# Kernel tuning notes

Hardware: AMD Instinct MI355X
Metric: run time of the kernel (lower is better)

Reference implementation:

```python
import jax, jax.numpy as jnp
import numpy as np

B, T, E, H = 4, 4096, 1024, 64

def setup_inputs() -> dict:
    key = jax.random.key(0)
    k1, k2, k3, k4 = jax.random.split(key, 4)
    embeddings = jax.random.normal(k1, (B, T, E), dtype=jnp.float32)
    Wq = jax.random.normal(k2, (H, E), dtype=jnp.float32) * (1.0 / np.sqrt(E))
    Wk = jax.random.normal(k3, (H, E), dtype=jnp.float32) * (1.0 / np.sqrt(E))
    Wv = jax.random.normal(k4, (H, E), dtype=jnp.float32) * (1.0 / np.sqrt(E))
    return {"embeddings": embeddings, "Wq": Wq, "Wk": Wk, "Wv": Wv}

def reference(embeddings, Wq, Wk, Wv):
    # Linear(E, H, bias=False): x @ W.T, W: [H, E]
    q = jnp.einsum('bte,he->bth', embeddings, Wq)  # [B,T,H]
    k = jnp.einsum('bte,he->bth', embeddings, Wk)  # [B,T,H]
    v = jnp.einsum('bte,he->bth', embeddings, Wv)  # [B,T,H]
    scale = embeddings.shape[-1] ** -0.5  # NOTE: source scales by embed_size**-0.5
    wei = jnp.einsum('bqh,bkh->bqk', q, k) * scale  # [B,T,T]
    Tn = embeddings.shape[1]
    causal = jnp.tril(jnp.ones((Tn, Tn), dtype=bool))
    wei = jnp.where(causal[None, :, :], wei, -jnp.inf)
    wei = jax.nn.softmax(wei, axis=-1)
    return jnp.einsum('bqk,bkh->bqh', wei, v)  # [B,T,H]
```

## Files before the change

### kernel.cpp

```cpp
#include <hip/hip_runtime.h>
#include <math.h>
#include <stdint.h>

#define BN 4
#define TN 4096
#define EN 1024
#define HN 64
#define BT (BN*TN)

typedef __attribute__((ext_vector_type(8))) short   short8;
typedef __attribute__((ext_vector_type(4))) float   f32x4;
typedef __attribute__((ext_vector_type(4))) unsigned short us4;
typedef __attribute__((ext_vector_type(8))) unsigned short us8;

__device__ __forceinline__ unsigned short f2b(float f) {
    union { float f; uint32_t u; } v; v.f = f;
    uint32_t u = v.u;
    return (unsigned short)((u + 0x7FFFu + ((u >> 16) & 1u)) >> 16);
}

__device__ __forceinline__ float fexp2(float x) {
#if __has_builtin(__builtin_amdgcn_exp2f)
    return __builtin_amdgcn_exp2f(x);
#else
    return exp2f(x);
#endif
}

__global__ __launch_bounds__(256)
void wconv(const float* __restrict__ Wq, const float* __restrict__ Wk,
           const float* __restrict__ Wv, unsigned short* __restrict__ W16) {
    const int row = blockIdx.x;
    const int t = threadIdx.x;
    const float* src;
    float sc = 1.0f;
    if (row < 64)       { src = Wq + (size_t)row * EN; sc = 0.045084220f; }
    else if (row < 128) { src = Wk + (size_t)(row - 64) * EN; }
    else                { src = Wv + (size_t)(row - 128) * EN; }
    float4 v = *(const float4*)(src + t * 4);
    us4 p;
    p[0] = f2b(v.x * sc); p[1] = f2b(v.y * sc);
    p[2] = f2b(v.z * sc); p[3] = f2b(v.w * sc);
    *(us4*)&W16[(size_t)row * EN + t * 4] = p;
}

__global__ __launch_bounds__(512, 2)
void qkv_gemm(const float* __restrict__ emb, const unsigned short* __restrict__ W16,
              unsigned short* __restrict__ QK, unsigned short* __restrict__ VT) {
    __shared__ __align__(16) unsigned short A_lds[2][64][72];
    __shared__ __align__(16) unsigned short B_lds[2][192][72];

    const int tid = threadIdx.x;
    const int wid = tid >> 6, lane = tid & 63;
    const int c = lane & 15, g = lane >> 4;
    const int wm = wid & 1, wn = wid >> 1;
    const int r0 = blockIdx.x * 64;

    const int ar = tid >> 3, ach = tid & 7;

    const f32x4 fzero = {0.f, 0.f, 0.f, 0.f};
    f32x4 acc[2][3];
    #pragma unroll
    for (int i = 0; i < 2; ++i)
        #pragma unroll
        for (int j = 0; j < 3; ++j) acc[i][j] = fzero;

    {
        float4 a0 = *(const float4*)&emb[(size_t)(r0 + ar) * EN + ach * 8];
        float4 a1 = *(const float4*)&emb[(size_t)(r0 + ar) * EN + ach * 8 + 4];
        us8 ap;
        ap[0] = f2b(a0.x); ap[1] = f2b(a0.y); ap[2] = f2b(a0.z); ap[3] = f2b(a0.w);
        ap[4] = f2b(a1.x); ap[5] = f2b(a1.y); ap[6] = f2b(a1.z); ap[7] = f2b(a1.w);
        *(us8*)&A_lds[0][ar][ach * 8] = ap;
        #pragma unroll
        for (int s = 0; s < 3; ++s) {
            const int f = tid + 512 * s;
            const int br = f >> 3, bch = f & 7;
            *(us8*)&B_lds[0][br][bch * 8] = *(const us8*)&W16[(size_t)br * EN + bch * 8];
        }
    }
    __syncthreads();

    for (int t = 0; t < 16; ++t) {
        const int cur = t & 1;
        const bool pf = (t < 15);
        const int kn = (t + 1) * 64;

        float4 a0, a1;
        us8 bw0, bw1, bw2;
        if (pf) {
            a0 = *(const float4*)&emb[(size_t)(r0 + ar) * EN + kn + ach * 8];
            a1 = *(const float4*)&emb[(size_t)(r0 + ar) * EN + kn + ach * 8 + 4];
            bw0 = *(const us8*)&W16[(size_t)((tid +    0) >> 3) * EN + kn + (tid & 7) * 8];
            bw1 = *(const us8*)&W16[(size_t)((tid +  512) >> 3) * EN + kn + ((tid + 512) & 7) * 8];
            bw2 = *(const us8*)&W16[(size_t)((tid + 1024) >> 3) * EN + kn + ((tid + 1024) & 7) * 8];
        }

        short8 af[2][2], bf[3][2];
        #pragma unroll
        for (int rt = 0; rt < 2; ++rt)
            #pragma unroll
            for (int ks = 0; ks < 2; ++ks)
                af[rt][ks] = *(const short8*)&A_lds[cur][32 * wm + 16 * rt + c][32 * ks + 8 * g];
        #pragma unroll
        for (int nt = 0; nt < 3; ++nt)
            #pragma unroll
            for (int ks = 0; ks < 2; ++ks)
                bf[nt][ks] = *(const short8*)&B_lds[cur][48 * wn + 16 * nt + c][32 * ks + 8 * g];
        #pragma unroll
        for (int ks = 0; ks < 2; ++ks)
            #pragma unroll
            for (int rt = 0; rt < 2; ++rt)
                #pragma unroll
                for (int nt = 0; nt < 3; ++nt)
                    acc[rt][nt] = __builtin_amdgcn_mfma_f32_16x16x32_bf16(
                        af[rt][ks], bf[nt][ks], acc[rt][nt], 0, 0, 0);

        if (pf) {
            us8 ap;
            ap[0] = f2b(a0.x); ap[1] = f2b(a0.y); ap[2] = f2b(a0.z); ap[3] = f2b(a0.w);
            ap[4] = f2b(a1.x); ap[5] = f2b(a1.y); ap[6] = f2b(a1.z); ap[7] = f2b(a1.w);
            *(us8*)&A_lds[cur ^ 1][ar][ach * 8] = ap;
            *(us8*)&B_lds[cur ^ 1][(tid +    0) >> 3][((tid +    0) & 7) * 8] = bw0;
            *(us8*)&B_lds[cur ^ 1][(tid +  512) >> 3][((tid +  512) & 7) * 8] = bw1;
            *(us8*)&B_lds[cur ^ 1][(tid + 1024) >> 3][((tid + 1024) & 7) * 8] = bw2;
        }
        __syncthreads();
    }

    #pragma unroll
    for (int rt = 0; rt < 2; ++rt) {
        #pragma unroll
        for (int nt = 0; nt < 3; ++nt) {
            const int n = 48 * wn + 16 * nt + c;
            const int wsel = n >> 6;
            const int d = n & 63;
            const int rbase = r0 + 32 * wm + 16 * rt + 4 * g;
            if (wsel < 2) {
                #pragma unroll
                for (int j = 0; j < 4; ++j)
                    QK[(size_t)wsel * BT * HN + (size_t)(rbase + j) * HN + d] =
                        f2b(acc[rt][nt][j]);
            } else {
                const int bb = rbase >> 12;
                const int tt = rbase & 4095;
                us4 p;
                #pragma unroll
                for (int j = 0; j < 4; ++j) p[j] = f2b(acc[rt][nt][j]);
                *(us4*)&VT[(size_t)bb * HN * TN + (size_t)d * TN + tt] = p;
            }
        }
    }
}

#define NW 4

__global__ __launch_bounds__(256, 2)
void attn(const unsigned short* __restrict__ QK,
          const unsigned short* __restrict__ VT, float* __restrict__ out) {
    __shared__ __align__(16) unsigned short KV[NW][2][64][72];
    __shared__ __align__(16) float MLm[NW][32];
    __shared__ __align__(16) float MLl[NW][32];
    __shared__ __align__(16) float ML2m[32];
    __shared__ __align__(16) float ML2l[32];

    const int tid = threadIdx.x;
    const int w = tid >> 6, lane = tid & 63, c = lane & 15, g = lane >> 4;
    const int bid = blockIdx.x;
    const int b = bid & 3;
    const int qt = (TN / 32 - 1) - (bid >> 2);

    const unsigned short* Qg = QK + ((size_t)b * TN + (size_t)qt * 32) * HN;
    const unsigned short* Kg = QK + (size_t)BT * HN + (size_t)b * TN * HN;
    const unsigned short* Vg = VT + (size_t)b * HN * TN;

    short8 bq[2][2];
    #pragma unroll
    for (int ct = 0; ct < 2; ++ct)
        #pragma unroll
        for (int ks = 0; ks < 2; ++ks)
            bq[ct][ks] = *(const short8*)&Qg[(size_t)(16 * ct + c) * HN + 32 * ks + 8 * g];

    const f32x4 fzero = {0.f, 0.f, 0.f, 0.f};
    f32x4 o[2][4];
    #pragma unroll
    for (int i = 0; i < 2; ++i)
        #pragma unroll
        for (int j = 0; j < 4; ++j) o[i][j] = fzero;
    float m[2] = {-INFINITY, -INFINITY};
    float l[2] = {0.f, 0.f};

    const int jmax = qt >> 1;
    unsigned short* Ks = &KV[w][0][0][0];
    unsigned short* Vs = &KV[w][1][0][0];

    for (int jt = w; jt <= jmax; jt += NW) {
        #pragma unroll
        for (int i = 0; i < 8; ++i) {
            const int f = lane + 64 * i;
            const int r = f >> 3, ch = f & 7;
            *(us8*)&Ks[r * 72 + ch * 8] =
                *(const us8*)&Kg[((size_t)jt * 64 + r) * HN + ch * 8];
        }
        #pragma unroll
        for (int i = 0; i < 8; ++i) {
            const int f = lane + 64 * i;
            const int r = f >> 3, ch = f & 7;
            *(us8*)&Vs[r * 72 + ch * 8] =
                *(const us8*)&Vg[(size_t)r * TN + (size_t)jt * 64 + ch * 8];
        }

        f32x4 st[4][2];
        #pragma unroll
        for (int kt = 0; kt < 4; ++kt)
            #pragma unroll
            for (int ct = 0; ct < 2; ++ct) st[kt][ct] = fzero;
        #pragma unroll
        for (int kt = 0; kt < 4; ++kt) {
            #pragma unroll
            for (int ks = 0; ks < 2; ++ks) {
                short8 ak = *(const short8*)&Ks[(16 * kt + c) * 72 + 32 * ks + 8 * g];
                #pragma unroll
                for (int ct = 0; ct < 2; ++ct)
                    st[kt][ct] = __builtin_amdgcn_mfma_f32_16x16x32_bf16(
                        ak, bq[ct][ks], st[kt][ct], 0, 0, 0);
            }
        }

        if (jt == jmax) {
            const int koff = jt * 64 - qt * 32;
            #pragma unroll
            for (int kt = 0; kt < 4; ++kt)
                #pragma unroll
                for (int ct = 0; ct < 2; ++ct)
                    #pragma unroll
                    for (int j = 0; j < 4; ++j)
                        if (16 * kt + 4 * g + j + koff > 16 * ct + c)
                            st[kt][ct][j] = -INFINITY;
        }

        #pragma unroll
        for (int ct = 0; ct < 2; ++ct) {
            float pmax = -INFINITY;
            #pragma unroll
            for (int kt = 0; kt < 4; ++kt)
                #pragma unroll
                for (int j = 0; j < 4; ++j) pmax = fmaxf(pmax, st[kt][ct][j]);
            pmax = fmaxf(pmax, __shfl_xor(pmax, 16));
            pmax = fmaxf(pmax, __shfl_xor(pmax, 32));
            const float mn = fmaxf(m[ct], pmax);
            const float alpha = fexp2(m[ct] - mn);
            float ls = 0.f;
            #pragma unroll
            for (int kt = 0; kt < 4; ++kt)
                #pragma unroll
                for (int j = 0; j < 4; ++j) {
                    float p = fexp2(st[kt][ct][j] - mn);
                    st[kt][ct][j] = p;
                    ls += p;
                }
            ls += __shfl_xor(ls, 16);
            ls += __shfl_xor(ls, 32);
            l[ct] = l[ct] * alpha + ls;
            m[ct] = mn;

            float a4[4];
            #pragma unroll
            for (int j = 0; j < 4; ++j) a4[j] = __shfl(alpha, 4 * g + j);
            #pragma unroll
            for (int dt = 0; dt < 4; ++dt)
                #pragma unroll
                for (int j = 0; j < 4; ++j) o[ct][dt][j] *= a4[j];
        }

        #pragma unroll
        for (int kt = 0; kt < 4; ++kt)
            #pragma unroll
            for (int ct = 0; ct < 2; ++ct) {
                us4 p;
                #pragma unroll
                for (int j = 0; j < 4; ++j) p[j] = f2b(st[kt][ct][j]);
                *(us4*)&Ks[(16 * ct + c) * 72 + 16 * kt + 4 * g] = p;
            }

        #pragma unroll
        for (int ks = 0; ks < 2; ++ks) {
            short8 pa[2];
            #pragma unroll
            for (int qp = 0; qp < 2; ++qp)
                pa[qp] = *(const short8*)&Ks[(16 * qp + c) * 72 + 32 * ks + 8 * g];
            #pragma unroll
            for (int dt = 0; dt < 4; ++dt) {
                short8 bv = *(const short8*)&Vs[(16 * dt + c) * 72 + 32 * ks + 8 * g];
                #pragma unroll
                for (int qp = 0; qp < 2; ++qp)
                    o[qp][dt] = __builtin_amdgcn_mfma_f32_16x16x32_bf16(
                        pa[qp], bv, o[qp][dt], 0, 0, 0);
            }
        }
    }

    if (g == 0) {
        MLm[w][c]      = m[0];  MLl[w][c]      = l[0];
        MLm[w][c + 16] = m[1];  MLl[w][c + 16] = l[1];
    }
    __syncthreads();

    if (tid < 32) {
        const int q = tid;
        float M = MLm[0][q];
        #pragma unroll
        for (int s = 1; s < NW; ++s) M = fmaxf(M, MLm[s][q]);
        float L = 0.f;
        #pragma unroll
        for (int s = 0; s < NW; ++s) L += MLl[s][q] * fexp2(MLm[s][q] - M);
        ML2m[q] = M;
        ML2l[q] = L;
    }
    __syncthreads();

    float* Oslab = (float*)&KV[0][0][0][0];
    float* Ow = Oslab + w * (32 * 65);
    #pragma unroll
    for (int qp = 0; qp < 2; ++qp) {
        float mo[4];
        #pragma unroll
        for (int j = 0; j < 4; ++j) mo[j] = __shfl(m[qp], 4 * g + j);
        #pragma unroll
        for (int j = 0; j < 4; ++j) {
            const int q = 16 * qp + 4 * g + j;
            const float sc = fexp2(mo[j] - ML2m[q]);
            #pragma unroll
            for (int dt = 0; dt < 4; ++dt)
                Ow[q * 65 + 16 * dt + c] = o[qp][dt][j] * sc;
        }
    }
    __syncthreads();

    const int d = 16 * w + c;
    #pragma unroll
    for (int tq = 0; tq < 8; ++tq) {
        const int q = 4 * tq + g;
        float v = 0.f;
        #pragma unroll
        for (int s = 0; s < NW; ++s) v += Oslab[s * (32 * 65) + q * 65 + d];
        out[((size_t)b * TN + (size_t)qt * 32 + q) * HN + d] = v / ML2l[q];
    }
}

extern "C" void kernel_launch(void* const* d_in, const int* in_sizes, int n_in,
                              void* d_out, int out_size, void* d_ws, size_t ws_size,
                              hipStream_t stream) {
    const float* emb = (const float*)d_in[0];
    const float* Wq  = (const float*)d_in[1];
    const float* Wk  = (const float*)d_in[2];
    const float* Wv  = (const float*)d_in[3];
    float* out = (float*)d_out;

    unsigned short* ws  = (unsigned short*)d_ws;
    unsigned short* W16 = ws;
    unsigned short* QK  = ws + 196608;
    unsigned short* VT  = ws + 196608 + 2 * (size_t)BT * HN;

    wconv<<<192, 256, 0, stream>>>(Wq, Wk, Wv, W16);
    qkv_gemm<<<BT / 64, 512, 0, stream>>>(emb, W16, QK, VT);
    attn<<<BN * (TN / 32), 256, 0, stream>>>(QK, VT, out);
}
```

Measured before the change: 144.2 us.

## Rewrite QKV GEMM as LDS-free register pipeline and shrink attention KV tiles

The QKV projection drops its shared-memory double buffering. Each wave now loads its A and B fragments straight from global memory into registers through a 4-deep prefetch ring, and each block covers 32 rows instead of 64, so the grid doubles. The attention kernel moves from 64-key to 32-key tiles with a smaller per-wave LDS slab and raises the occupancy hint to 4 blocks per CU. It also adds lazy softmax rescaling: the running max and output rescale are skipped while the new max stays within 8 (log2 units) of the old one. This trades redundant global loads in the GEMM and more, smaller attention iterations for less LDS traffic and higher occupancy.

```diff
diff --git a/kernel.cpp b/kernel.cpp
--- a/kernel.cpp
+++ b/kernel.cpp
@@ -44,121 +44,90 @@
     *(us4*)&W16[(size_t)row * EN + t * 4] = p;
 }
 
-__global__ __launch_bounds__(512, 2)
+__global__ __launch_bounds__(512)
 void qkv_gemm(const float* __restrict__ emb, const unsigned short* __restrict__ W16,
               unsigned short* __restrict__ QK, unsigned short* __restrict__ VT) {
-    __shared__ __align__(16) unsigned short A_lds[2][64][72];
-    __shared__ __align__(16) unsigned short B_lds[2][192][72];
-
     const int tid = threadIdx.x;
     const int wid = tid >> 6, lane = tid & 63;
     const int c = lane & 15, g = lane >> 4;
     const int wm = wid & 1, wn = wid >> 1;
-    const int r0 = blockIdx.x * 64;
-
-    const int ar = tid >> 3, ach = tid & 7;
+    const int r0 = blockIdx.x * 32;
+
+    const float* aptr = emb + (size_t)(r0 + 16 * wm + c) * EN + 8 * g;
+    const unsigned short* bptr0 = W16 + (size_t)(48 * wn + c) * EN + 8 * g;
+    const unsigned short* bptr1 = bptr0 + (size_t)16 * EN;
+    const unsigned short* bptr2 = bptr0 + (size_t)32 * EN;
 
     const f32x4 fzero = {0.f, 0.f, 0.f, 0.f};
-    f32x4 acc[2][3];
-    #pragma unroll
-    for (int i = 0; i < 2; ++i)
-        #pragma unroll
-        for (int j = 0; j < 3; ++j) acc[i][j] = fzero;
-
-    {
-        float4 a0 = *(const float4*)&emb[(size_t)(r0 + ar) * EN + ach * 8];
-        float4 a1 = *(const float4*)&emb[(size_t)(r0 + ar) * EN + ach * 8 + 4];
-        us8 ap;
-        ap[0] = f2b(a0.x); ap[1] = f2b(a0.y); ap[2] = f2b(a0.z); ap[3] = f2b(a0.w);
-        ap[4] = f2b(a1.x); ap[5] = f2b(a1.y); ap[6] = f2b(a1.z); ap[7] = f2b(a1.w);
-        *(us8*)&A_lds[0][ar][ach * 8] = ap;
-        #pragma unroll
-        for (int s = 0; s < 3; ++s) {
-            const int f = tid + 512 * s;
-            const int br = f >> 3, bch = f & 7;
-            *(us8*)&B_lds[0][br][bch * 8] = *(const us8*)&W16[(size_t)br * EN + bch * 8];
-        }
-    }
-    __syncthreads();
-
-    for (int t = 0; t < 16; ++t) {
-        const int cur = t & 1;
-        const bool pf = (t < 15);
-        const int kn = (t + 1) * 64;
-
-        float4 a0, a1;
-        us8 bw0, bw1, bw2;
-        if (pf) {
-            a0 = *(const float4*)&emb[(size_t)(r0 + ar) * EN + kn + ach * 8];
-            a1 = *(const float4*)&emb[(size_t)(r0 + ar) * EN + kn + ach * 8 + 4];
-            bw0 = *(const us8*)&W16[(size_t)((tid +    0) >> 3) * EN + kn + (tid & 7) * 8];
-            bw1 = *(const us8*)&W16[(size_t)((tid +  512) >> 3) * EN + kn + ((tid + 512) & 7) * 8];
-            bw2 = *(const us8*)&W16[(size_t)((tid + 1024) >> 3) * EN + kn + ((tid + 1024) & 7) * 8];
-        }
-
-        short8 af[2][2], bf[3][2];
-        #pragma unroll
-        for (int rt = 0; rt < 2; ++rt)
-            #pragma unroll
-            for (int ks = 0; ks < 2; ++ks)
-                af[rt][ks] = *(const short8*)&A_lds[cur][32 * wm + 16 * rt + c][32 * ks + 8 * g];
-        #pragma unroll
-        for (int nt = 0; nt < 3; ++nt)
-            #pragma unroll
-            for (int ks = 0; ks < 2; ++ks)
-                bf[nt][ks] = *(const short8*)&B_lds[cur][48 * wn + 16 * nt + c][32 * ks + 8 * g];
-        #pragma unroll
-        for (int ks = 0; ks < 2; ++ks)
-            #pragma unroll
-            for (int rt = 0; rt < 2; ++rt)
-                #pragma unroll
-                for (int nt = 0; nt < 3; ++nt)
-                    acc[rt][nt] = __builtin_amdgcn_mfma_f32_16x16x32_bf16(
-                        af[rt][ks], bf[nt][ks], acc[rt][nt], 0, 0, 0);
-
-        if (pf) {
-            us8 ap;
-            ap[0] = f2b(a0.x); ap[1] = f2b(a0.y); ap[2] = f2b(a0.z); ap[3] = f2b(a0.w);
-            ap[4] = f2b(a1.x); ap[5] = f2b(a1.y); ap[6] = f2b(a1.z); ap[7] = f2b(a1.w);
-            *(us8*)&A_lds[cur ^ 1][ar][ach * 8] = ap;
-            *(us8*)&B_lds[cur ^ 1][(tid +    0) >> 3][((tid +    0) & 7) * 8] = bw0;
-            *(us8*)&B_lds[cur ^ 1][(tid +  512) >> 3][((tid +  512) & 7) * 8] = bw1;
-            *(us8*)&B_lds[cur ^ 1][(tid + 1024) >> 3][((tid + 1024) & 7) * 8] = bw2;
-        }
-        __syncthreads();
-    }
-
-    #pragma unroll
-    for (int rt = 0; rt < 2; ++rt) {
-        #pragma unroll
-        for (int nt = 0; nt < 3; ++nt) {
-            const int n = 48 * wn + 16 * nt + c;
-            const int wsel = n >> 6;
-            const int d = n & 63;
-            const int rbase = r0 + 32 * wm + 16 * rt + 4 * g;
-            if (wsel < 2) {
-                #pragma unroll
-                for (int j = 0; j < 4; ++j)
-                    QK[(size_t)wsel * BT * HN + (size_t)(rbase + j) * HN + d] =
-                        f2b(acc[rt][nt][j]);
-            } else {
-                const int bb = rbase >> 12;
-                const int tt = rbase & 4095;
-                us4 p;
-                #pragma unroll
-                for (int j = 0; j < 4; ++j) p[j] = f2b(acc[rt][nt][j]);
-                *(us4*)&VT[(size_t)bb * HN * TN + (size_t)d * TN + tt] = p;
-            }
+    f32x4 acc[3];
+    #pragma unroll
+    for (int j = 0; j < 3; ++j) acc[j] = fzero;
+
+    float4 a0[4], a1[4];
+    us8 b0[4], b1[4], b2[4];
+
+    #pragma unroll
+    for (int t = 0; t < 4; ++t) {
+        a0[t] = *(const float4*)(aptr + 32 * t);
+        a1[t] = *(const float4*)(aptr + 32 * t + 4);
+        b0[t] = *(const us8*)(bptr0 + 32 * t);
+        b1[t] = *(const us8*)(bptr1 + 32 * t);
+        b2[t] = *(const us8*)(bptr2 + 32 * t);
+    }
+
+    #pragma unroll 4
+    for (int t = 0; t < 32; ++t) {
+        const int cur = t & 3;
+        us8 af;
+        af[0] = f2b(a0[cur].x); af[1] = f2b(a0[cur].y);
+        af[2] = f2b(a0[cur].z); af[3] = f2b(a0[cur].w);
+        af[4] = f2b(a1[cur].x); af[5] = f2b(a1[cur].y);
+        af[6] = f2b(a1[cur].z); af[7] = f2b(a1[cur].w);
+        const short8 afs = *(const short8*)&af;
+        acc[0] = __builtin_amdgcn_mfma_f32_16x16x32_bf16(afs, *(const short8*)&b0[cur], acc[0], 0, 0, 0);
+        acc[1] = __builtin_amdgcn_mfma_f32_16x16x32_bf16(afs, *(const short8*)&b1[cur], acc[1], 0, 0, 0);
+        acc[2] = __builtin_amdgcn_mfma_f32_16x16x32_bf16(afs, *(const short8*)&b2[cur], acc[2], 0, 0, 0);
+        if (t + 4 < 32) {
+            const int kn = 32 * (t + 4);
+            a0[cur] = *(const float4*)(aptr + kn);
+            a1[cur] = *(const float4*)(aptr + kn + 4);
+            b0[cur] = *(const us8*)(bptr0 + kn);
+            b1[cur] = *(const us8*)(bptr1 + kn);
+            b2[cur] = *(const us8*)(bptr2 + kn);
+        }
+    }
+
+    #pragma unroll
+    for (int nt = 0; nt < 3; ++nt) {
+        const int n = 48 * wn + 16 * nt + c;
+        const int wsel = n >> 6;
+        const int d = n & 63;
+        const int rbase = r0 + 16 * wm + 4 * g;
+        if (wsel < 2) {
+            #pragma unroll
+            for (int j = 0; j < 4; ++j)
+                QK[(size_t)wsel * BT * HN + (size_t)(rbase + j) * HN + d] =
+                    f2b(acc[nt][j]);
+        } else {
+            const int bb = rbase >> 12;
+            const int tt = rbase & 4095;
+            us4 p;
+            #pragma unroll
+            for (int j = 0; j < 4; ++j) p[j] = f2b(acc[nt][j]);
+            *(us4*)&VT[(size_t)bb * HN * TN + (size_t)d * TN + tt] = p;
         }
     }
 }
 
 #define NW 4
-
-__global__ __launch_bounds__(256, 2)
+#define KSLOT 2304
+#define VSLOT 2560
+#define WSLOT (KSLOT+VSLOT)
+
+__global__ __launch_bounds__(256, 4)
 void attn(const unsigned short* __restrict__ QK,
           const unsigned short* __restrict__ VT, float* __restrict__ out) {
-    __shared__ __align__(16) unsigned short KV[NW][2][64][72];
+    __shared__ __align__(16) unsigned short SLAB[NW * WSLOT];
     __shared__ __align__(16) float MLm[NW][32];
     __shared__ __align__(16) float MLl[NW][32];
     __shared__ __align__(16) float ML2m[32];
@@ -174,6 +143,9 @@
     const unsigned short* Kg = QK + (size_t)BT * HN + (size_t)b * TN * HN;
     const unsigned short* Vg = VT + (size_t)b * HN * TN;
 
+    unsigned short* Ks = SLAB + w * WSLOT;
+    unsigned short* Vs = Ks + KSLOT;
+
     short8 bq[2][2];
     #pragma unroll
     for (int ct = 0; ct < 2; ++ct)
@@ -190,33 +162,27 @@
     float m[2] = {-INFINITY, -INFINITY};
     float l[2] = {0.f, 0.f};
 
-    const int jmax = qt >> 1;
-    unsigned short* Ks = &KV[w][0][0][0];
-    unsigned short* Vs = &KV[w][1][0][0];
-
-    for (int jt = w; jt <= jmax; jt += NW) {
-        #pragma unroll
-        for (int i = 0; i < 8; ++i) {
+    for (int jt = w; jt <= qt; jt += NW) {
+        #pragma unroll
+        for (int i = 0; i < 4; ++i) {
             const int f = lane + 64 * i;
-            const int r = f >> 3, ch = f & 7;
-            *(us8*)&Ks[r * 72 + ch * 8] =
-                *(const us8*)&Kg[((size_t)jt * 64 + r) * HN + ch * 8];
-        }
-        #pragma unroll
-        for (int i = 0; i < 8; ++i) {
+            *(us8*)&Ks[(f >> 3) * 72 + (f & 7) * 8] =
+                *(const us8*)&Kg[((size_t)jt * 32 + (f >> 3)) * HN + (f & 7) * 8];
+        }
+        #pragma unroll
+        for (int i = 0; i < 4; ++i) {
             const int f = lane + 64 * i;
-            const int r = f >> 3, ch = f & 7;
-            *(us8*)&Vs[r * 72 + ch * 8] =
-                *(const us8*)&Vg[(size_t)r * TN + (size_t)jt * 64 + ch * 8];
-        }
-
-        f32x4 st[4][2];
-        #pragma unroll
-        for (int kt = 0; kt < 4; ++kt)
+            *(us8*)&Vs[(f >> 2) * 40 + (f & 3) * 8] =
+                *(const us8*)&Vg[(size_t)(f >> 2) * TN + (size_t)jt * 32 + (f & 3) * 8];
+        }
+
+        f32x4 st[2][2];
+        #pragma unroll
+        for (int kt = 0; kt < 2; ++kt)
             #pragma unroll
             for (int ct = 0; ct < 2; ++ct) st[kt][ct] = fzero;
         #pragma unroll
-        for (int kt = 0; kt < 4; ++kt) {
+        for (int kt = 0; kt < 2; ++kt) {
             #pragma unroll
             for (int ks = 0; ks < 2; ++ks) {
                 short8 ak = *(const short8*)&Ks[(16 * kt + c) * 72 + 32 * ks + 8 * g];
@@ -227,15 +193,14 @@
             }
         }
 
-        if (jt == jmax) {
-            const int koff = jt * 64 - qt * 32;
-            #pragma unroll
-            for (int kt = 0; kt < 4; ++kt)
+        if (jt == qt) {
+            #pragma unroll
+            for (int kt = 0; kt < 2; ++kt)
                 #pragma unroll
                 for (int ct = 0; ct < 2; ++ct)
                     #pragma unroll
                     for (int j = 0; j < 4; ++j)
-                        if (16 * kt + 4 * g + j + koff > 16 * ct + c)
+                        if (16 * kt + 4 * g + j > 16 * ct + c)
                             st[kt][ct][j] = -INFINITY;
         }
 
@@ -243,16 +208,29 @@
         for (int ct = 0; ct < 2; ++ct) {
             float pmax = -INFINITY;
             #pragma unroll
-            for (int kt = 0; kt < 4; ++kt)
+            for (int kt = 0; kt < 2; ++kt)
                 #pragma unroll
                 for (int j = 0; j < 4; ++j) pmax = fmaxf(pmax, st[kt][ct][j]);
             pmax = fmaxf(pmax, __shfl_xor(pmax, 16));
             pmax = fmaxf(pmax, __shfl_xor(pmax, 32));
-            const float mn = fmaxf(m[ct], pmax);
-            const float alpha = fexp2(m[ct] - mn);
+            float mn = m[ct];
+            float alpha = 1.f;
+            const bool defer = __all(pmax - m[ct] <= 8.0f);
+            if (!defer) {
+                mn = fmaxf(m[ct], pmax);
+                alpha = fexp2(m[ct] - mn);
+                float a4[4];
+                #pragma unroll
+                for (int j = 0; j < 4; ++j) a4[j] = __shfl(alpha, 4 * g + j);
+                #pragma unroll
+                for (int dt = 0; dt < 4; ++dt)
+                    #pragma unroll
+                    for (int j = 0; j < 4; ++j) o[ct][dt][j] *= a4[j];
+                m[ct] = mn;
+            }
             float ls = 0.f;
             #pragma unroll
-            for (int kt = 0; kt < 4; ++kt)
+            for (int kt = 0; kt < 2; ++kt)
                 #pragma unroll
                 for (int j = 0; j < 4; ++j) {
                     float p = fexp2(st[kt][ct][j] - mn);
@@ -262,19 +240,10 @@
             ls += __shfl_xor(ls, 16);
             ls += __shfl_xor(ls, 32);
             l[ct] = l[ct] * alpha + ls;
-            m[ct] = mn;
-
-            float a4[4];
-            #pragma unroll
-            for (int j = 0; j < 4; ++j) a4[j] = __shfl(alpha, 4 * g + j);
-            #pragma unroll
-            for (int dt = 0; dt < 4; ++dt)
-                #pragma unroll
-                for (int j = 0; j < 4; ++j) o[ct][dt][j] *= a4[j];
-        }
-
-        #pragma unroll
-        for (int kt = 0; kt < 4; ++kt)
+        }
+
+        #pragma unroll
+        for (int kt = 0; kt < 2; ++kt)
             #pragma unroll
             for (int ct = 0; ct < 2; ++ct) {
                 us4 p;
@@ -283,19 +252,14 @@
                 *(us4*)&Ks[(16 * ct + c) * 72 + 16 * kt + 4 * g] = p;
             }
 
-        #pragma unroll
-        for (int ks = 0; ks < 2; ++ks) {
-            short8 pa[2];
-            #pragma unroll
-            for (int qp = 0; qp < 2; ++qp)
-                pa[qp] = *(const short8*)&Ks[(16 * qp + c) * 72 + 32 * ks + 8 * g];
+        {
+            short8 pa0 = *(const short8*)&Ks[(c) * 72 + 8 * g];
+            short8 pa1 = *(const short8*)&Ks[(16 + c) * 72 + 8 * g];
             #pragma unroll
             for (int dt = 0; dt < 4; ++dt) {
-                short8 bv = *(const short8*)&Vs[(16 * dt + c) * 72 + 32 * ks + 8 * g];
-                #pragma unroll
-                for (int qp = 0; qp < 2; ++qp)
-                    o[qp][dt] = __builtin_amdgcn_mfma_f32_16x16x32_bf16(
-                        pa[qp], bv, o[qp][dt], 0, 0, 0);
+                short8 bv = *(const short8*)&Vs[(16 * dt + c) * 40 + 8 * g];
+                o[0][dt] = __builtin_amdgcn_mfma_f32_16x16x32_bf16(pa0, bv, o[0][dt], 0, 0, 0);
+                o[1][dt] = __builtin_amdgcn_mfma_f32_16x16x32_bf16(pa1, bv, o[1][dt], 0, 0, 0);
             }
         }
     }
@@ -319,8 +283,8 @@
     }
     __syncthreads();
 
-    float* Oslab = (float*)&KV[0][0][0][0];
-    float* Ow = Oslab + w * (32 * 65);
+    float* Oslab = (float*)SLAB;
+    float* Ow = Oslab + (size_t)w * (32 * 65);
     #pragma unroll
     for (int qp = 0; qp < 2; ++qp) {
         float mo[4];
@@ -343,7 +307,7 @@
         const int q = 4 * tq + g;
         float v = 0.f;
         #pragma unroll
-        for (int s = 0; s < NW; ++s) v += Oslab[s * (32 * 65) + q * 65 + d];
+        for (int s = 0; s < NW; ++s) v += Oslab[(size_t)s * (32 * 65) + q * 65 + d];
         out[((size_t)b * TN + (size_t)qt * 32 + q) * HN + d] = v / ML2l[q];
     }
 }
@@ -363,6 +327,6 @@
     unsigned short* VT  = ws + 196608 + 2 * (size_t)BT * HN;
 
     wconv<<<192, 256, 0, stream>>>(Wq, Wk, Wv, W16);
-    qkv_gemm<<<BT / 64, 512, 0, stream>>>(emb, W16, QK, VT);
+    qkv_gemm<<<BT / 32, 512, 0, stream>>>(emb, W16, QK, VT);
     attn<<<BN * (TN / 32), 256, 0, stream>>>(QK, VT, out);
 }
```

Result: slower. 264.6 us (+83.5%).
